# Optimization experiments

Measured on AMD Instinct MI355X. Metric: run time of the kernel, lower is better.

The kernel has to match this reference:

```python
import jax, jax.numpy as jnp
import numpy as np

B, S = 4096, 128
POS_RANK, DIR_RANK = 10, 4
WIDTH = 256
POS_DIM = POS_RANK * 6  # 60
DIR_DIM = DIR_RANK * 6  # 24
SKIPS = (4,)


def _pe(x, rank):
    # x: [N, 3] -> [N, 6*rank]; sin/cos of x scaled by 2^i for i in 0..rank-1
    freqs = (2.0 ** jnp.arange(rank)).astype(x.dtype)        # [L]
    xf = x[..., None] * freqs                                 # [N, 3, L]
    enc = jnp.concatenate([jnp.sin(xf), jnp.cos(xf)], axis=-1)  # [N, 3, 2L]
    return enc.reshape(x.shape[0], -1)


def _linear_init(key, fan_in, fan_out):
    k1, k2 = jax.random.split(key)
    bound = 1.0 / np.sqrt(fan_in)
    W = jax.random.uniform(k1, (fan_in, fan_out), jnp.float32, -bound, bound)
    b = jax.random.uniform(k2, (fan_out,), jnp.float32, -bound, bound)
    return W, b


def setup_inputs() -> dict:
    key = jax.random.key(0)
    ks = jax.random.split(key, 16)
    inp = {
        "input_pos": jax.random.normal(ks[0], (B, S, 3), jnp.float32),
        "input_dir": jax.random.normal(ks[1], (B, S, 3), jnp.float32),
    }
    # trunk layers: in-dims follow skip-concat structure
    in_dims = [POS_DIM] + [WIDTH + POS_DIM if (i in SKIPS) else WIDTH for i in range(7)]
    for i, d_in in enumerate(in_dims):
        W, b = _linear_init(ks[2 + i], d_in, WIDTH)
        inp[f"W{i}"] = W
        inp[f"b{i}"] = b
    inp["Wd"], inp["bd"] = _linear_init(ks[10], WIDTH, 1)
    inp["Wc0"], inp["bc0"] = _linear_init(ks[11], WIDTH + DIR_DIM, WIDTH // 2)
    inp["Wc1"], inp["bc1"] = _linear_init(ks[12], WIDTH // 2, 3)
    return inp


def reference(input_pos, input_dir,
              W0, b0, W1, b1, W2, b2, W3, b3, W4, b4, W5, b5, W6, b6, W7, b7,
              Wd, bd, Wc0, bc0, Wc1, bc1):
    Ws = [W0, W1, W2, W3, W4, W5, W6, W7]
    bs = [b0, b1, b2, b3, b4, b5, b6, b7]
    b, s, _ = input_pos.shape
    embed_pos = _pe(input_pos.reshape(-1, 3), POS_RANK)  # [N, 60]
    embed_dir = _pe(input_dir.reshape(-1, 3), DIR_RANK)  # [N, 24]
    hx = embed_pos
    for i, (W, bb) in enumerate(zip(Ws, bs)):
        hx = jax.nn.relu(hx @ W + bb)
        if i in SKIPS:
            hx = jnp.concatenate([hx, embed_pos], axis=1)
    density = (hx @ Wd + bd).reshape(b, s)
    dir_feat = jnp.concatenate([hx, embed_dir], axis=1)  # [N, 280]
    color = (jax.nn.relu(dir_feat @ Wc0 + bc0) @ Wc1 + bc1).reshape(b, s, 3)
    return density, color
```

## Files before the change

kernel.cpp:

```cpp
#include <hip/hip_runtime.h>
#include <hip/hip_bf16.h>

using bf16 = __bf16;
typedef __bf16 bf16x8 __attribute__((ext_vector_type(8)));
typedef __bf16 bf16x4 __attribute__((ext_vector_type(4)));
typedef float  f32x4  __attribute__((ext_vector_type(4)));

#define MFMA16(a, b, c) __builtin_amdgcn_mfma_f32_16x16x32_bf16((a), (b), (c), 0, 0, 0)

constexpr int P0  = 0;
constexpr int P1  = 16384;
constexpr int P2  = 81920;
constexpr int P3  = 147456;
constexpr int P4  = 212992;
constexpr int P5  = 278528;
constexpr int P6  = 360448;
constexpr int P7  = 425984;
constexpr int PD  = 491520;
constexpr int PC0 = 495616;
constexpr int PC1 = 532480;

constexpr int NPTS = 4096 * 128;
constexpr int SH = 328;

struct PackArgs {
    const float* src[11];
    int K[11], N[11], Ntiles[11], tasks[11], dstoff[11];
};

__global__ void nerf_pack(PackArgs pa, bf16* __restrict__ dst) {
    int idx = blockIdx.x * 256 + threadIdx.x;
    for (int l = 0; l < 11; ++l) {
        if (idx < pa.tasks[l]) {
            const int lane = idx & 63;
            const int blk  = idx >> 6;
            const int nt   = blk % pa.Ntiles[l];
            const int kt   = blk / pa.Ntiles[l];
            const int kb   = kt * 32 + (lane >> 4) * 8;
            const int n    = nt * 16 + (lane & 15);
            const float* s = pa.src[l];
            const int K = pa.K[l], N = pa.N[l];
            bf16x8 v;
#pragma unroll
            for (int j = 0; j < 8; ++j) {
                int k = kb + j;
                v[j] = (bf16)((k < K && n < N) ? s[(size_t)k * N + n] : 0.f);
            }
            *(bf16x8*)(dst + pa.dstoff[l] + (size_t)idx * 8) = v;
            return;
        }
        idx -= pa.tasks[l];
    }
}

template <int KP, int N, bool RELU, int MODE, bool HAZARD>
__device__ __forceinline__ void layer(const bf16* src, bf16* H,
                                      const bf16* __restrict__ wp,
                                      const float* __restrict__ bias,
                                      float* __restrict__ gout, int m0) {
    constexpr int NTILES = N / 16;
    constexpr int NT_W   = (NTILES < 8) ? NTILES : 8;
    constexpr int CG     = NTILES / NT_W;
    constexpr int NPG    = 2 / CG;
    constexpr int PT_W   = 4 / NPG;

    const int tid  = threadIdx.x;
    const int lane = tid & 63;
    const int w    = tid >> 6;
    const int l15  = lane & 15;
    const int quad = lane >> 4;
    const int nt0  = (w % CG) * NT_W;
    const int pt0  = (w / CG) * PT_W;

    f32x4 acc[PT_W][NT_W];
    if constexpr (MODE == 0) {
#pragma unroll
        for (int nt = 0; nt < NT_W; ++nt) {
            f32x4 b4 = *(const f32x4*)(bias + (nt0 + nt) * 16 + quad * 4);
#pragma unroll
            for (int pt = 0; pt < PT_W; ++pt) acc[pt][nt] = b4;
        }
    } else if constexpr (MODE == 1) {
        const float bv = bias[0];
        f32x4 t = {bv, bv, bv, bv};
#pragma unroll
        for (int pt = 0; pt < PT_W; ++pt) acc[pt][0] = t;
    } else {
        f32x4 t = {bias[0], bias[1], bias[2], 0.f};
#pragma unroll
        for (int pt = 0; pt < PT_W; ++pt) acc[pt][0] = t;
    }

#pragma unroll 2
    for (int kt = 0; kt < KP / 32; ++kt) {
        bf16x8 wf[NT_W];
#pragma unroll
        for (int nt = 0; nt < NT_W; ++nt)
            wf[nt] = *(const bf16x8*)(wp + ((size_t)(kt * NTILES + nt0 + nt) * 64 + lane) * 8);
#pragma unroll
        for (int pt = 0; pt < PT_W; ++pt) {
            const int point = (pt0 + pt) * 16 + l15;
            bf16x8 af = *(const bf16x8*)(src + point * SH + kt * 32 + quad * 8);
#pragma unroll
            for (int nt = 0; nt < NT_W; ++nt)
                acc[pt][nt] = MFMA16(wf[nt], af, acc[pt][nt]);
        }
    }
    if (HAZARD) __syncthreads();

    if constexpr (MODE == 0) {
#pragma unroll
        for (int pt = 0; pt < PT_W; ++pt) {
            const int point = (pt0 + pt) * 16 + l15;
#pragma unroll
            for (int nt = 0; nt < NT_W; ++nt) {
                f32x4 a = acc[pt][nt];
                bf16x4 o;
#pragma unroll
                for (int r = 0; r < 4; ++r) {
                    float v = a[r];
                    if (RELU) v = v > 0.f ? v : 0.f;
                    o[r] = (bf16)v;
                }
                *(bf16x4*)(H + point * SH + (nt0 + nt) * 16 + quad * 4) = o;
            }
        }
        __syncthreads();
    } else if constexpr (MODE == 1) {
        if (quad == 0) {
#pragma unroll
            for (int pt = 0; pt < PT_W; ++pt)
                gout[m0 + (pt0 + pt) * 16 + l15] = acc[pt][0][0];
        }
    } else {
        if (quad == 0) {
#pragma unroll
            for (int pt = 0; pt < PT_W; ++pt) {
                const size_t p3 = (size_t)(m0 + (pt0 + pt) * 16 + l15) * 3;
                gout[p3 + 0] = acc[pt][0][0];
                gout[p3 + 1] = acc[pt][0][1];
                gout[p3 + 2] = acc[pt][0][2];
            }
        }
    }
}

__global__ __launch_bounds__(128, 2)
void nerf_main(const float* __restrict__ pos, const float* __restrict__ dir,
               const float* __restrict__ b0, const float* __restrict__ b1,
               const float* __restrict__ b2, const float* __restrict__ b3,
               const float* __restrict__ b4, const float* __restrict__ b5,
               const float* __restrict__ b6, const float* __restrict__ b7,
               const float* __restrict__ bd, const float* __restrict__ bc0,
               const float* __restrict__ bc1,
               const bf16* __restrict__ wpk, float* __restrict__ out) {
    __shared__ __align__(16) bf16 H[64 * SH];

    const int m0 = blockIdx.x * 64;
    const int tid = threadIdx.x;

    *(unsigned int*)(H + (tid & 63) * SH + 316 + 2 * (tid >> 6)) = 0u;

    {
        const int row  = tid >> 1;
        const int half = tid & 1;
        const size_t pb = (size_t)(m0 + row) * 3;
        float xs[3] = { pos[pb], pos[pb + 1], pos[pb + 2] };
#pragma unroll
        for (int j = 0; j < 30; ++j) {
            const int col = half * 30 + j;
            const int c = col / 20, rem = col % 20, s = rem / 10, i = rem % 10;
            const float arg = xs[c] * (float)(1 << i);
            float v = s ? __cosf(arg) : __sinf(arg);
            H[row * SH + 256 + col] = (bf16)v;
        }
    }
    __syncthreads();

    layer<64,  256, true, 0, false>(H + 256, H, wpk + P0, b0, nullptr, m0);
    layer<256, 256, true, 0, true >(H, H, wpk + P1, b1, nullptr, m0);
    layer<256, 256, true, 0, true >(H, H, wpk + P2, b2, nullptr, m0);
    layer<256, 256, true, 0, true >(H, H, wpk + P3, b3, nullptr, m0);
    layer<256, 256, true, 0, true >(H, H, wpk + P4, b4, nullptr, m0);
    layer<320, 256, true, 0, true >(H, H, wpk + P5, b5, nullptr, m0);
    layer<256, 256, true, 0, true >(H, H, wpk + P6, b6, nullptr, m0);
    layer<256, 256, true, 0, true >(H, H, wpk + P7, b7, nullptr, m0);

    layer<256, 16, false, 1, false>(H, H, wpk + PD, bd, out, m0);

    {
        const int row  = tid >> 1;
        const int half = tid & 1;
        const size_t db = (size_t)(m0 + row) * 3;
        float ds[3] = { dir[db], dir[db + 1], dir[db + 2] };
#pragma unroll
        for (int j = 0; j < 12; ++j) {
            const int col = half * 12 + j;
            const int c = col / 8, rem = col % 8, s = rem / 4, i = rem % 4;
            const float arg = ds[c] * (float)(1 << i);
            float v = s ? __cosf(arg) : __sinf(arg);
            H[row * SH + 256 + col] = (bf16)v;
        }
        *(unsigned long long*)(H + row * SH + 280 + half * 4) = 0ull;
    }
    __syncthreads();

    layer<288, 128, true, 0, true >(H, H, wpk + PC0, bc0, nullptr, m0);
    layer<128, 16, false, 2, false>(H, H, wpk + PC1, bc1, out + NPTS, m0);
}

__global__ void nerf_sentinel(float* __restrict__ out, float val) {
    if (threadIdx.x == 0 && blockIdx.x == 0) out[0] = val;
}

extern "C" void kernel_launch(void* const* d_in, const int* in_sizes, int n_in,
                              void* d_out, int out_size, void* d_ws, size_t ws_size,
                              hipStream_t stream) {
    static const int exp2[24] = {
        1572864, 1572864,
        15360, 256, 65536, 256, 65536, 256, 65536, 256,
        65536, 256, 80896, 256, 65536, 256, 65536, 256,
        256, 1, 35840, 128, 384, 3
    };
    int bad = -1;
    if (n_in != 24) bad = 99;
    else {
        for (int i = 0; i < 24; ++i)
            if (in_sizes[i] != exp2[i]) { bad = i; break; }
    }
    if (bad < 0 && out_size != NPTS * 4) bad = 97;
    if (bad >= 0) {
        nerf_sentinel<<<1, 64, 0, stream>>>((float*)d_out, 20000.f + 100.f * bad);
        return;
    }

    static const int wi[11] = {2, 4, 6, 8, 10, 12, 14, 16, 18, 20, 22};
    static const int Ks[11] = {60, 256, 256, 256, 256, 316, 256, 256, 256, 280, 128};
    static const int Ns[11] = {256, 256, 256, 256, 256, 256, 256, 256, 1, 128, 3};
    static const int Kp[11] = {64, 256, 256, 256, 256, 320, 256, 256, 256, 288, 128};
    static const int Np[11] = {256, 256, 256, 256, 256, 256, 256, 256, 16, 128, 16};

    PackArgs pa;
    int off = 0, total_tasks = 0;
    for (int l = 0; l < 11; ++l) {
        pa.src[l]    = (const float*)d_in[wi[l]];
        pa.K[l]      = Ks[l];
        pa.N[l]      = Ns[l];
        pa.Ntiles[l] = Np[l] / 16;
        pa.tasks[l]  = (Kp[l] / 32) * (Np[l] / 16) * 64;
        pa.dstoff[l] = off;
        off += pa.tasks[l] * 8;
        total_tasks += pa.tasks[l];
    }
    bf16* wpk = (bf16*)d_ws;

    nerf_pack<<<(total_tasks + 255) / 256, 256, 0, stream>>>(pa, wpk);

    nerf_main<<<NPTS / 64, 128, 0, stream>>>(
        (const float*)d_in[0], (const float*)d_in[1],
        (const float*)d_in[3], (const float*)d_in[5], (const float*)d_in[7],
        (const float*)d_in[9], (const float*)d_in[11], (const float*)d_in[13],
        (const float*)d_in[15], (const float*)d_in[17], (const float*)d_in[19],
        (const float*)d_in[21], (const float*)d_in[23],
        wpk, (float*)d_out);
}
```

Baseline: 645.3 us.

## Split each 64-point block across eight waves instead of two

Raises the block size from 128 to 512 threads and redistributes the MLP layer tiles so each wave computes only two 16-column output tiles instead of eight, with predication for waves that have no point tiles in narrow layers. The positional-encoding prologues are spread over eight threads per point, and padding columns are written as zeros inline. The intent is more waves in flight per CU to hide LDS and weight-load latency and to cut per-wave register pressure. The cost is that each wave now loads the same A fragments for every column group, weight fragments are reused over fewer MFMAs, and most waves sit idle in the narrow density and color layers.

```diff
diff --git a/kernel.cpp b/kernel.cpp
--- a/kernel.cpp
+++ b/kernel.cpp
@@ -58,11 +58,13 @@
                                       const bf16* __restrict__ wp,
                                       const float* __restrict__ bias,
                                       float* __restrict__ gout, int m0) {
+    constexpr int NW     = 8;
     constexpr int NTILES = N / 16;
-    constexpr int NT_W   = (NTILES < 8) ? NTILES : 8;
+    constexpr int NT_W   = (NTILES >= 16) ? 2 : ((NTILES >= 8) ? 2 : 1);
     constexpr int CG     = NTILES / NT_W;
-    constexpr int NPG    = 2 / CG;
-    constexpr int PT_W   = 4 / NPG;
+    static_assert(CG <= NW && NW % CG == 0, "wave split");
+    constexpr int NPG    = NW / CG;
+    constexpr int PT_W   = (4 + NPG - 1) / NPG;
 
     const int tid  = threadIdx.x;
     const int lane = tid & 63;
@@ -71,81 +73,93 @@
     const int quad = lane >> 4;
     const int nt0  = (w % CG) * NT_W;
     const int pt0  = (w / CG) * PT_W;
+    const bool active = (pt0 < 4);
 
     f32x4 acc[PT_W][NT_W];
+    if (active) {
+        if constexpr (MODE == 0) {
+#pragma unroll
+            for (int nt = 0; nt < NT_W; ++nt) {
+                f32x4 b4 = *(const f32x4*)(bias + (nt0 + nt) * 16 + quad * 4);
+#pragma unroll
+                for (int pt = 0; pt < PT_W; ++pt) acc[pt][nt] = b4;
+            }
+        } else if constexpr (MODE == 1) {
+            const float bv = bias[0];
+            f32x4 t = {bv, bv, bv, bv};
+#pragma unroll
+            for (int pt = 0; pt < PT_W; ++pt) acc[pt][0] = t;
+        } else {
+            f32x4 t = {bias[0], bias[1], bias[2], 0.f};
+#pragma unroll
+            for (int pt = 0; pt < PT_W; ++pt) acc[pt][0] = t;
+        }
+
+#pragma unroll 2
+        for (int kt = 0; kt < KP / 32; ++kt) {
+            bf16x8 wf[NT_W];
+#pragma unroll
+            for (int nt = 0; nt < NT_W; ++nt)
+                wf[nt] = *(const bf16x8*)(wp + ((size_t)(kt * NTILES + nt0 + nt) * 64 + lane) * 8);
+#pragma unroll
+            for (int pt = 0; pt < PT_W; ++pt) {
+                if (pt0 + pt < 4) {
+                    const int point = (pt0 + pt) * 16 + l15;
+                    bf16x8 af = *(const bf16x8*)(src + point * SH + kt * 32 + quad * 8);
+#pragma unroll
+                    for (int nt = 0; nt < NT_W; ++nt)
+                        acc[pt][nt] = MFMA16(wf[nt], af, acc[pt][nt]);
+                }
+            }
+        }
+    }
+    if (HAZARD) __syncthreads();
+
     if constexpr (MODE == 0) {
-#pragma unroll
-        for (int nt = 0; nt < NT_W; ++nt) {
-            f32x4 b4 = *(const f32x4*)(bias + (nt0 + nt) * 16 + quad * 4);
-#pragma unroll
-            for (int pt = 0; pt < PT_W; ++pt) acc[pt][nt] = b4;
-        }
-    } else if constexpr (MODE == 1) {
-        const float bv = bias[0];
-        f32x4 t = {bv, bv, bv, bv};
-#pragma unroll
-        for (int pt = 0; pt < PT_W; ++pt) acc[pt][0] = t;
-    } else {
-        f32x4 t = {bias[0], bias[1], bias[2], 0.f};
-#pragma unroll
-        for (int pt = 0; pt < PT_W; ++pt) acc[pt][0] = t;
-    }
-
-#pragma unroll 2
-    for (int kt = 0; kt < KP / 32; ++kt) {
-        bf16x8 wf[NT_W];
-#pragma unroll
-        for (int nt = 0; nt < NT_W; ++nt)
-            wf[nt] = *(const bf16x8*)(wp + ((size_t)(kt * NTILES + nt0 + nt) * 64 + lane) * 8);
-#pragma unroll
-        for (int pt = 0; pt < PT_W; ++pt) {
-            const int point = (pt0 + pt) * 16 + l15;
-            bf16x8 af = *(const bf16x8*)(src + point * SH + kt * 32 + quad * 8);
-#pragma unroll
-            for (int nt = 0; nt < NT_W; ++nt)
-                acc[pt][nt] = MFMA16(wf[nt], af, acc[pt][nt]);
-        }
-    }
-    if (HAZARD) __syncthreads();
-
-    if constexpr (MODE == 0) {
-#pragma unroll
-        for (int pt = 0; pt < PT_W; ++pt) {
-            const int point = (pt0 + pt) * 16 + l15;
-#pragma unroll
-            for (int nt = 0; nt < NT_W; ++nt) {
-                f32x4 a = acc[pt][nt];
-                bf16x4 o;
-#pragma unroll
-                for (int r = 0; r < 4; ++r) {
-                    float v = a[r];
-                    if (RELU) v = v > 0.f ? v : 0.f;
-                    o[r] = (bf16)v;
+        if (active) {
+#pragma unroll
+            for (int pt = 0; pt < PT_W; ++pt) {
+                if (pt0 + pt < 4) {
+                    const int point = (pt0 + pt) * 16 + l15;
+#pragma unroll
+                    for (int nt = 0; nt < NT_W; ++nt) {
+                        f32x4 a = acc[pt][nt];
+                        bf16x4 o;
+#pragma unroll
+                        for (int r = 0; r < 4; ++r) {
+                            float v = a[r];
+                            if (RELU) v = v > 0.f ? v : 0.f;
+                            o[r] = (bf16)v;
+                        }
+                        *(bf16x4*)(H + point * SH + (nt0 + nt) * 16 + quad * 4) = o;
+                    }
                 }
-                *(bf16x4*)(H + point * SH + (nt0 + nt) * 16 + quad * 4) = o;
             }
         }
         __syncthreads();
     } else if constexpr (MODE == 1) {
-        if (quad == 0) {
+        if (active && quad == 0) {
 #pragma unroll
             for (int pt = 0; pt < PT_W; ++pt)
-                gout[m0 + (pt0 + pt) * 16 + l15] = acc[pt][0][0];
+                if (pt0 + pt < 4)
+                    gout[m0 + (pt0 + pt) * 16 + l15] = acc[pt][0][0];
         }
     } else {
-        if (quad == 0) {
+        if (active && quad == 0) {
 #pragma unroll
             for (int pt = 0; pt < PT_W; ++pt) {
-                const size_t p3 = (size_t)(m0 + (pt0 + pt) * 16 + l15) * 3;
-                gout[p3 + 0] = acc[pt][0][0];
-                gout[p3 + 1] = acc[pt][0][1];
-                gout[p3 + 2] = acc[pt][0][2];
-            }
-        }
-    }
-}
-
-__global__ __launch_bounds__(128, 2)
+                if (pt0 + pt < 4) {
+                    const size_t p3 = (size_t)(m0 + (pt0 + pt) * 16 + l15) * 3;
+                    gout[p3 + 0] = acc[pt][0][0];
+                    gout[p3 + 1] = acc[pt][0][1];
+                    gout[p3 + 2] = acc[pt][0][2];
+                }
+            }
+        }
+    }
+}
+
+__global__ __launch_bounds__(512, 6)
 void nerf_main(const float* __restrict__ pos, const float* __restrict__ dir,
                const float* __restrict__ b0, const float* __restrict__ b1,
                const float* __restrict__ b2, const float* __restrict__ b3,
@@ -159,19 +173,20 @@
     const int m0 = blockIdx.x * 64;
     const int tid = threadIdx.x;
 
-    *(unsigned int*)(H + (tid & 63) * SH + 316 + 2 * (tid >> 6)) = 0u;
-
     {
-        const int row  = tid >> 1;
-        const int half = tid & 1;
+        const int row = tid >> 3;
+        const int oct = tid & 7;
         const size_t pb = (size_t)(m0 + row) * 3;
         float xs[3] = { pos[pb], pos[pb + 1], pos[pb + 2] };
 #pragma unroll
-        for (int j = 0; j < 30; ++j) {
-            const int col = half * 30 + j;
-            const int c = col / 20, rem = col % 20, s = rem / 10, i = rem % 10;
-            const float arg = xs[c] * (float)(1 << i);
-            float v = s ? __cosf(arg) : __sinf(arg);
+        for (int j = 0; j < 8; ++j) {
+            const int col = oct * 8 + j;
+            float v = 0.f;
+            if (col < 60) {
+                const int c = col / 20, rem = col % 20, s = rem / 10, i = rem % 10;
+                const float arg = xs[c] * (float)(1 << i);
+                v = s ? __cosf(arg) : __sinf(arg);
+            }
             H[row * SH + 256 + col] = (bf16)v;
         }
     }
@@ -189,19 +204,21 @@
     layer<256, 16, false, 1, false>(H, H, wpk + PD, bd, out, m0);
 
     {
-        const int row  = tid >> 1;
-        const int half = tid & 1;
+        const int row = tid >> 3;
+        const int oct = tid & 7;
         const size_t db = (size_t)(m0 + row) * 3;
         float ds[3] = { dir[db], dir[db + 1], dir[db + 2] };
 #pragma unroll
-        for (int j = 0; j < 12; ++j) {
-            const int col = half * 12 + j;
-            const int c = col / 8, rem = col % 8, s = rem / 4, i = rem % 4;
-            const float arg = ds[c] * (float)(1 << i);
-            float v = s ? __cosf(arg) : __sinf(arg);
+        for (int j = 0; j < 4; ++j) {
+            const int col = oct * 4 + j;
+            float v = 0.f;
+            if (col < 24) {
+                const int c = col / 8, rem = col % 8, s = rem / 4, i = rem % 4;
+                const float arg = ds[c] * (float)(1 << i);
+                v = s ? __cosf(arg) : __sinf(arg);
+            }
             H[row * SH + 256 + col] = (bf16)v;
         }
-        *(unsigned long long*)(H + row * SH + 280 + half * 4) = 0ull;
     }
     __syncthreads();
 
@@ -256,7 +273,7 @@
 
     nerf_pack<<<(total_tasks + 255) / 256, 256, 0, stream>>>(pa, wpk);
 
-    nerf_main<<<NPTS / 64, 128, 0, stream>>>(
+    nerf_main<<<NPTS / 64, 512, 0, stream>>>(
         (const float*)d_in[0], (const float*)d_in[1],
         (const float*)d_in[3], (const float*)d_in[5], (const float*)d_in[7],
         (const float*)d_in[9], (const float*)d_in[11], (const float*)d_in[13],
```

Result: faster. 621.9 us (-3.6%).
